# Kernel tuning notes

Hardware: AMD Instinct MI355X
Metric: run time of the kernel (lower is better)

Reference implementation:

```python
import jax, jax.numpy as jnp
import numpy as np

B = 64        # batch_size (rejection-sampling proposals per column)
P = 200000    # p (number of spike-and-slab variables)
K = 10        # number of accepted samples kept per column
ZETA = 1.1
GAMMA = -0.1
BETA = 2.0 / 3.0
GZ_LOGRATIO = -GAMMA / ZETA


def setup_inputs() -> dict:
    key = jax.random.key(0)
    kZ, kU, ku = jax.random.split(key, 3)
    return {
        "Z": jax.random.normal(kZ, (B, P), dtype=jnp.float32),
        "U": jax.random.uniform(kU, (B, P), dtype=jnp.float32),
        "u": jax.random.uniform(ku, (K, P), dtype=jnp.float32),
        "gamma_alpha": jnp.ones((P,), dtype=jnp.float32),
        "logalpha": jnp.ones((P,), dtype=jnp.float32),
        "batch_size": B,
    }


def reference(Z, U, u, gamma_alpha, logalpha, batch_size):
    # --- MarsagliaTsampler ---
    alpha = jax.nn.relu(gamma_alpha) + 1.0          # [P]
    d = alpha - 1.0 / 3.0                            # [P]
    c = 1.0 / jnp.sqrt(9.0 * d)                      # [P]
    V = (1.0 + c * Z) ** 3                           # [B, P]
    cond1 = Z > -1.0 / c
    cond2 = jnp.log(U) < 0.5 * Z ** 2 + d - d * V + d * jnp.log(V)
    cond = cond1 & cond2                             # nan comparisons -> False, as in torch
    out = jnp.where(cond, d * V, 0.0)                # [B, P]
    # take the FIRST K accepted samples per column (stable compaction)
    order = jnp.where(cond, jnp.arange(batch_size)[:, None], batch_size)
    idx = jnp.argsort(order, axis=0)[:K]             # [K, P]
    theta = jnp.take_along_axis(out, idx, axis=0)    # [K, P]

    # --- hard-concrete spike-and-slab gate (training mode) ---
    z_mean = jax.nn.sigmoid(logalpha - BETA * GZ_LOGRATIO)          # [P]
    s = jax.nn.sigmoid((jnp.log(u) - jnp.log1p(-u) + logalpha) / BETA)  # [K, P]
    z = jnp.clip((ZETA - GAMMA) * s + GAMMA, 0.0, 1.0)              # [K, P]

    return z, z_mean, theta, alpha, logalpha
```

## Files before the change

### kernel.cpp

```cpp
#include <hip/hip_runtime.h>
#include <math.h>

#define KACC 10
#define CH1 12
#define CH2 8

__global__ __launch_bounds__(256)
void sss_kernel(const float* __restrict__ Z, const float* __restrict__ U,
                const float* __restrict__ uu, const float* __restrict__ ga,
                const float* __restrict__ la, float* __restrict__ out,
                int P, int B, int nbScan, int perK, int vec4)
{
#pragma clang fp contract(off)
    const size_t KP = (size_t)KACC * (size_t)P;
    float* o_z        = out;
    float* o_zmean    = out + KP;
    float* o_theta    = out + KP + (size_t)P;
    float* o_alpha    = out + 2 * KP + (size_t)P;
    float* o_logalpha = out + 2 * KP + 2 * (size_t)P;

    const int bid = blockIdx.x;

    if (bid < nbScan) {
        const int p = bid * blockDim.x + threadIdx.x;
        if (p >= P) return;

        const float g = ga[p];
        const float alpha = fmaxf(g, 0.0f) + 1.0f;
        const float d     = alpha - (1.0f / 3.0f);
        const float c     = 1.0f / sqrtf(9.0f * d);
        const float neg_inv_c = -(1.0f / c);

        float th[KACC];
#pragma unroll
        for (int k = 0; k < KACC; ++k) th[k] = 0.0f;
        int cnt = 0;

        {
            float zv[CH1], wv[CH1];
#pragma unroll
            for (int i = 0; i < CH1; ++i) {
                const size_t off = (size_t)i * (size_t)P + (size_t)p;
                zv[i] = Z[off];
                wv[i] = U[off];
            }
#pragma unroll
            for (int i = 0; i < CH1; ++i) {
                float z  = zv[i];
                float Uv = wv[i];
                float t  = 1.0f + c * z;
                float V  = (t * t) * t;
                float rhs = ((0.5f * (z * z) + d) - d * V) + d * logf(V);
                bool acc = (z > neg_inv_c) && (logf(Uv) < rhs) && (cnt < KACC);
                float val = d * V;
#pragma unroll
                for (int k = 0; k < KACC; ++k)
                    th[k] = (acc && cnt == k) ? val : th[k];
                cnt += acc ? 1 : 0;
            }
        }

        if (cnt < KACC) {
            for (int base = CH1; base < B; base += CH2) {
                float zv[CH2], wv[CH2];
#pragma unroll
                for (int i = 0; i < CH2; ++i) {
                    const int r = base + i;
                    const size_t off = (size_t)r * (size_t)P + (size_t)p;
                    zv[i] = (r < B) ? Z[off] : __int_as_float(0x7fc00000);
                    wv[i] = (r < B) ? U[off] : 1.0f;
                }
#pragma unroll
                for (int i = 0; i < CH2; ++i) {
                    float z  = zv[i];
                    float Uv = wv[i];
                    float t  = 1.0f + c * z;
                    float V  = (t * t) * t;
                    float rhs = ((0.5f * (z * z) + d) - d * V) + d * logf(V);
                    bool acc = (z > neg_inv_c) && (logf(Uv) < rhs) && (cnt < KACC);
                    float val = d * V;
#pragma unroll
                    for (int k = 0; k < KACC; ++k)
                        th[k] = (acc && cnt == k) ? val : th[k];
                    cnt += acc ? 1 : 0;
                }
                if (cnt >= KACC) break;
            }
        }

#pragma unroll
        for (int k = 0; k < KACC; ++k)
            o_theta[(size_t)k * (size_t)P + (size_t)p] = th[k];
        o_alpha[p] = alpha;

    } else {
        const int gb  = bid - nbScan;
        const int k   = gb / perK;
        const int blk = gb - k * perK;
        const float SHIFT = 0.060606062f;

        if (vec4) {
            const int P4 = P >> 2;
            const int i4 = blk * blockDim.x + threadIdx.x;
            if (i4 >= P4) return;

            const float4 u4  = reinterpret_cast<const float4*>(uu + (size_t)k * (size_t)P)[i4];
            const float4 la4 = reinterpret_cast<const float4*>(la)[i4];

            float4 z4;
            {
                const float* us = (const float*)&u4;
                const float* ls = (const float*)&la4;
                float* zs = (float*)&z4;
#pragma unroll
                for (int j = 0; j < 4; ++j) {
                    float x = ((__logf(us[j]) - __logf(1.0f - us[j])) + ls[j]) * 1.5f;
                    float s = 1.0f / (1.0f + __expf(-x));
                    float zz = 1.2f * s - 0.1f;
                    zs[j] = fminf(fmaxf(zz, 0.0f), 1.0f);
                }
            }
            reinterpret_cast<float4*>(o_z + (size_t)k * (size_t)P)[i4] = z4;

            if (k == 0) {
                const float* ls = (const float*)&la4;
                float4 zm4;
                float* zm = (float*)&zm4;
#pragma unroll
                for (int j = 0; j < 4; ++j)
                    zm[j] = 1.0f / (1.0f + __expf(-(ls[j] - SHIFT)));
                reinterpret_cast<float4*>(o_zmean)[i4]    = zm4;
                reinterpret_cast<float4*>(o_logalpha)[i4] = la4;
            }
        } else {
            const int p = blk * blockDim.x + threadIdx.x;
            if (p >= P) return;
            const float u = uu[(size_t)k * (size_t)P + (size_t)p];
            const float lalpha = la[p];
            float x = ((__logf(u) - __logf(1.0f - u)) + lalpha) * 1.5f;
            float s = 1.0f / (1.0f + __expf(-x));
            float zz = 1.2f * s - 0.1f;
            o_z[(size_t)k * (size_t)P + (size_t)p] = fminf(fmaxf(zz, 0.0f), 1.0f);
            if (k == 0) {
                o_zmean[p]    = 1.0f / (1.0f + __expf(-(lalpha - SHIFT)));
                o_logalpha[p] = lalpha;
            }
        }
    }
}

extern "C" void kernel_launch(void* const* d_in, const int* in_sizes, int n_in,
                              void* d_out, int out_size, void* d_ws, size_t ws_size,
                              hipStream_t stream) {
    const float* Z  = (const float*)d_in[0];
    const float* U  = (const float*)d_in[1];
    const float* uu = (const float*)d_in[2];
    const float* ga = (const float*)d_in[3];
    const float* la = (const float*)d_in[4];
    float* out = (float*)d_out;

    const int P = in_sizes[3];
    const int B = in_sizes[0] / P;
    const int K = in_sizes[2] / P;

    const int block  = 256;
    const int nbScan = (P + block - 1) / block;
    const int vec4   = (P % 4 == 0) ? 1 : 0;
    const int perK   = vec4 ? ((P / 4 + block - 1) / block)
                            : ((P + block - 1) / block);
    const int grid   = nbScan + K * perK;
    sss_kernel<<<grid, block, 0, stream>>>(Z, U, uu, ga, la, out, P, B, nbScan, perK, vec4);
}
```

Before: 19.64 us.

## Split rejection-sampler rows across four wave groups with shared-memory compaction

Each scan block now covers 64 columns instead of 256. Four row groups of 64 threads each evaluate 3 of the first 12 proposal rows in parallel and write accept bits and candidate values to LDS. After a barrier, only the first wave compacts the first K accepted values and continues the serial scan for the remaining rows if needed. The aim is to spread the transcendental work on the first rows over more threads and raise parallelism. In exchange it adds a block barrier and shared-memory traffic, leaves three quarters of each block idle after the barrier, and uses 4x more scan blocks.

```diff
diff --git a/kernel.cpp b/kernel.cpp
--- a/kernel.cpp
+++ b/kernel.cpp
@@ -2,8 +2,9 @@
 #include <math.h>
 
 #define KACC 10
-#define CH1 12
-#define CH2 8
+#define NRG 4
+#define RPG 3
+#define SCOLS 64
 
 __global__ __launch_bounds__(256)
 void sss_kernel(const float* __restrict__ Z, const float* __restrict__ U,
@@ -22,60 +23,84 @@
     const int bid = blockIdx.x;
 
     if (bid < nbScan) {
-        const int p = bid * blockDim.x + threadIdx.x;
-        if (p >= P) return;
-
-        const float g = ga[p];
+        __shared__ float s_val[NRG * RPG][SCOLS];
+        __shared__ int   s_msk[NRG][SCOLS];
+
+        const int t    = threadIdx.x;
+        const int lane = t & (SCOLS - 1);
+        const int rg   = t >> 6;
+        const int col  = bid * SCOLS + lane;
+        const bool cok = (col < P);
+
+        const float g = cok ? ga[col] : 1.0f;
         const float alpha = fmaxf(g, 0.0f) + 1.0f;
         const float d     = alpha - (1.0f / 3.0f);
         const float c     = 1.0f / sqrtf(9.0f * d);
         const float neg_inv_c = -(1.0f / c);
 
+        {
+            float zv[RPG], wv[RPG];
+#pragma unroll
+            for (int j = 0; j < RPG; ++j) {
+                const int row = rg * RPG + j;
+                const size_t off = (size_t)row * (size_t)P + (size_t)col;
+                const bool ok = cok && (row < B);
+                zv[j] = ok ? Z[off] : __int_as_float(0x7fc00000);
+                wv[j] = ok ? U[off] : 1.0f;
+            }
+            int m = 0;
+#pragma unroll
+            for (int j = 0; j < RPG; ++j) {
+                float z  = zv[j];
+                float Uv = wv[j];
+                float tt = 1.0f + c * z;
+                float V  = (tt * tt) * tt;
+                float rhs = ((0.5f * (z * z) + d) - d * V) + d * logf(V);
+                bool acc = (z > neg_inv_c) && (logf(Uv) < rhs);
+                m |= acc ? (1 << j) : 0;
+                s_val[rg * RPG + j][lane] = d * V;
+            }
+            s_msk[rg][lane] = m;
+        }
+        __syncthreads();
+        if (rg != 0) return;
+
+        const int mask = s_msk[0][lane]
+                       | (s_msk[1][lane] << RPG)
+                       | (s_msk[2][lane] << (2 * RPG))
+                       | (s_msk[3][lane] << (3 * RPG));
+
         float th[KACC];
 #pragma unroll
         for (int k = 0; k < KACC; ++k) th[k] = 0.0f;
         int cnt = 0;
-
-        {
-            float zv[CH1], wv[CH1];
-#pragma unroll
-            for (int i = 0; i < CH1; ++i) {
-                const size_t off = (size_t)i * (size_t)P + (size_t)p;
-                zv[i] = Z[off];
-                wv[i] = U[off];
-            }
-#pragma unroll
-            for (int i = 0; i < CH1; ++i) {
-                float z  = zv[i];
-                float Uv = wv[i];
-                float t  = 1.0f + c * z;
-                float V  = (t * t) * t;
-                float rhs = ((0.5f * (z * z) + d) - d * V) + d * logf(V);
-                bool acc = (z > neg_inv_c) && (logf(Uv) < rhs) && (cnt < KACC);
-                float val = d * V;
-#pragma unroll
-                for (int k = 0; k < KACC; ++k)
-                    th[k] = (acc && cnt == k) ? val : th[k];
-                cnt += acc ? 1 : 0;
-            }
+#pragma unroll
+        for (int j = 0; j < NRG * RPG; ++j) {
+            bool acc = ((mask >> j) & 1) && (cnt < KACC);
+            float val = s_val[j][lane];
+#pragma unroll
+            for (int k = 0; k < KACC; ++k)
+                th[k] = (acc && cnt == k) ? val : th[k];
+            cnt += acc ? 1 : 0;
         }
 
         if (cnt < KACC) {
-            for (int base = CH1; base < B; base += CH2) {
-                float zv[CH2], wv[CH2];
-#pragma unroll
-                for (int i = 0; i < CH2; ++i) {
-                    const int r = base + i;
-                    const size_t off = (size_t)r * (size_t)P + (size_t)p;
-                    zv[i] = (r < B) ? Z[off] : __int_as_float(0x7fc00000);
-                    wv[i] = (r < B) ? U[off] : 1.0f;
+            for (int base = NRG * RPG; base < B; base += 4) {
+                float zv[4], wv[4];
+#pragma unroll
+                for (int i = 0; i < 4; ++i) {
+                    const int row = base + i;
+                    const size_t off = (size_t)row * (size_t)P + (size_t)col;
+                    const bool ok = cok && (row < B);
+                    zv[i] = ok ? Z[off] : __int_as_float(0x7fc00000);
+                    wv[i] = ok ? U[off] : 1.0f;
                 }
 #pragma unroll
-                for (int i = 0; i < CH2; ++i) {
+                for (int i = 0; i < 4; ++i) {
                     float z  = zv[i];
                     float Uv = wv[i];
-                    float t  = 1.0f + c * z;
-                    float V  = (t * t) * t;
+                    float tt = 1.0f + c * z;
+                    float V  = (tt * tt) * tt;
                     float rhs = ((0.5f * (z * z) + d) - d * V) + d * logf(V);
                     bool acc = (z > neg_inv_c) && (logf(Uv) < rhs) && (cnt < KACC);
                     float val = d * V;
@@ -88,10 +113,12 @@
             }
         }
 
-#pragma unroll
-        for (int k = 0; k < KACC; ++k)
-            o_theta[(size_t)k * (size_t)P + (size_t)p] = th[k];
-        o_alpha[p] = alpha;
+        if (cok) {
+#pragma unroll
+            for (int k = 0; k < KACC; ++k)
+                o_theta[(size_t)k * (size_t)P + (size_t)col] = th[k];
+            o_alpha[col] = alpha;
+        }
 
     } else {
         const int gb  = bid - nbScan;
@@ -164,7 +191,7 @@
     const int K = in_sizes[2] / P;
 
     const int block  = 256;
-    const int nbScan = (P + block - 1) / block;
+    const int nbScan = (P + SCOLS - 1) / SCOLS;
     const int vec4   = (P % 4 == 0) ? 1 : 0;
     const int perK   = vec4 ? ((P / 4 + block - 1) / block)
                             : ((P + block - 1) / block);
```

After: 16.51 us. -15.9%, faster.
